# Kernel tuning notes

Measured on AMD Instinct MI355X. Metric: run time of the kernel, lower is better.

## Reference

```python
import jax, jax.numpy as jnp
import numpy as np

DEPTH, DIM, HEADS, DH, MLP, N, B = 6, 192, 12, 16, 768, 256, 32
INNER = HEADS * DH  # 192


def setup_inputs() -> dict:
    key = jax.random.key(0)
    ks = jax.random.split(key, 10)
    w = lambda i, shape: jax.random.normal(ks[i], shape, dtype=jnp.float32) * 0.02
    return {
        'x': jax.random.normal(ks[0], (B, N, DIM), dtype=jnp.float32),
        'ln1_g': jnp.ones((DEPTH, DIM), jnp.float32),
        'ln1_b': jnp.zeros((DEPTH, DIM), jnp.float32),
        'Wq': w(1, (DEPTH, DIM, INNER)),
        'Wkv': w(2, (DEPTH, DIM, 2 * INNER)),
        'lsa_scale': jnp.full((DEPTH, HEADS), DH ** -0.5, dtype=jnp.float32),
        'mix_pre': jax.random.normal(ks[3], (DEPTH, HEADS, HEADS), dtype=jnp.float32),
        'mix_post': jax.random.normal(ks[4], (DEPTH, HEADS, HEADS), dtype=jnp.float32),
        'Wo': w(5, (DEPTH, INNER, DIM)),
        'bo': jnp.zeros((DEPTH, DIM), jnp.float32),
        'ls1': jnp.full((DEPTH, DIM), 0.1, dtype=jnp.float32),
        'ln2_g': jnp.ones((DEPTH, DIM), jnp.float32),
        'ln2_b': jnp.zeros((DEPTH, DIM), jnp.float32),
        'W1': w(6, (DEPTH, DIM, MLP)),
        'b1': jnp.zeros((DEPTH, MLP), jnp.float32),
        'W2': w(7, (DEPTH, MLP, DIM)),
        'b2': jnp.zeros((DEPTH, DIM), jnp.float32),
        'ls2': jnp.full((DEPTH, DIM), 0.1, dtype=jnp.float32),
    }


def _ln(x, g, b, eps=1e-5):
    m = x.mean(-1, keepdims=True)
    v = ((x - m) ** 2).mean(-1, keepdims=True)
    return (x - m) * jax.lax.rsqrt(v + eps) * g + b


def _heads(t, b, n):
    # (b, n, h*d) -> (b, h, n, d)
    return t.reshape(b, n, HEADS, DH).transpose(0, 2, 1, 3)


def _forward(x, ln1_g, ln1_b, Wq, Wkv, lsa_scale, mix_pre, mix_post, Wo, bo,
             ls1, ln2_g, ln2_b, W1, b1, W2, b2, ls2):
    b, n, _ = x.shape
    diag = jnp.arange(n)
    for l in range(DEPTH):
        # --- PreNorm + talking-heads LSA attention + LayerScale(0.1) ---
        h = _ln(x, ln1_g[l], ln1_b[l])
        q = _heads(h @ Wq[l], b, n)
        k, v = jnp.split(h @ Wkv[l], 2, axis=-1)
        k, v = _heads(k, b, n), _heads(v, b, n)
        dots = jnp.einsum('bhid,bhjd->bhij', q, k) * lsa_scale[l][None, :, None, None]
        # LSA: source sets diagonal to -1e-09 (literal, near-zero) when if_patch_attn
        dots = dots.at[:, :, diag, diag].set(-1e-9)
        dots = jnp.einsum('bhij,hg->bgij', dots, mix_pre[l])
        a = jax.nn.softmax(dots, axis=-1)
        a = jnp.einsum('bhij,hg->bgij', a, mix_post[l])
        o = jnp.einsum('bhij,bhjd->bhid', a, v)
        o = o.transpose(0, 2, 1, 3).reshape(b, n, INNER) @ Wo[l] + bo[l]
        x = x + o * ls1[l]
        # --- PreNorm + GELU FFN + LayerScale(0.1) ---
        h2 = _ln(x, ln2_g[l], ln2_b[l])
        f = jax.nn.gelu(h2 @ W1[l] + b1[l], approximate=False) @ W2[l] + b2[l]
        x = x + f * ls2[l]
    return x


def reference(x, ln1_g, ln1_b, Wq, Wkv, lsa_scale, mix_pre, mix_post, Wo, bo,
              ls1, ln2_g, ln2_b, W1, b1, W2, b2, ls2):
    return _forward(x, ln1_g, ln1_b, Wq, Wkv, lsa_scale, mix_pre, mix_post, Wo,
                    bo, ls1, ln2_g, ln2_b, W1, b1, W2, b2, ls2)
```

## Files before the change

### kernel.cpp

```cpp
#include <hip/hip_runtime.h>
#include <hip/hip_bf16.h>

#define DEPTH   6
#define DIM     192
#define HEADS   12
#define DH      16
#define MLPD    768
#define SEQ     256
#define BATCH   32
#define ROWS    (BATCH*SEQ)

typedef __attribute__((ext_vector_type(8))) short short8;
typedef __attribute__((ext_vector_type(4))) float f32x4;
typedef __attribute__((ext_vector_type(4))) _Float16 half4;
typedef __attribute__((ext_vector_type(8))) _Float16 half8;
typedef __hip_bfloat16 bf16_t;
typedef _Float16 f16_t;

__device__ __forceinline__ bf16_t f2b(float v){ return __float2bfloat16(v); }
__device__ __forceinline__ ushort f2u(float v){
    union{ bf16_t b; ushort u; } w; w.b = __float2bfloat16(v); return w.u;
}
__device__ __forceinline__ f16_t u2h(ushort u){ union{ ushort u; f16_t h; } w; w.u = u; return w.h; }
__device__ __forceinline__ ushort h2u(f16_t h){ union{ ushort u; f16_t h; } w; w.h = h; return w.u; }

__device__ __forceinline__ void async16(ushort* lds, const ushort* gp){
    __builtin_amdgcn_global_load_lds(
        (const __attribute__((address_space(1))) uint*)gp,
        (__attribute__((address_space(3))) uint*)lds, 16, 0, 0);
}

__global__ void copy_kernel(const float* __restrict__ x, float* __restrict__ xr, int n){
    int i = blockIdx.x*256 + threadIdx.x;
    if (i < n) xr[i] = x[i];
}

__device__ __forceinline__ void wt_tile(const float* __restrict__ W,
        ushort* __restrict__ WT, int K, int N, int l, int tx, int ty,
        int tid, ushort* T){
    const float* src = W + ((size_t)l*K + tx*64)*N + ty*64;
    ushort* dst = WT + ((size_t)l*N + ty*64)*K + tx*64;
    int r = tid >> 2, c4 = (tid & 3)*16;
    #pragma unroll
    for (int u=0; u<4; u++){
        float4 v = *(const float4*)(src + (size_t)r*N + c4 + u*4);
        T[(c4+u*4+0)*72 + r] = f2u(v.x);
        T[(c4+u*4+1)*72 + r] = f2u(v.y);
        T[(c4+u*4+2)*72 + r] = f2u(v.z);
        T[(c4+u*4+3)*72 + r] = f2u(v.w);
    }
    __syncthreads();
    int n = tid >> 2, k8 = (tid & 3)*16;
    #pragma unroll
    for (int u=0; u<2; u++)
        *(uint4*)(dst + (size_t)n*K + k8 + u*8) = *(uint4*)&T[n*72 + k8 + u*8];
}

__global__ __launch_bounds__(256) void wt_all(
        const float* __restrict__ Wq, const float* __restrict__ Wkv,
        const float* __restrict__ Wo, const float* __restrict__ W1,
        const float* __restrict__ W2,
        ushort* __restrict__ WqT, ushort* __restrict__ WkvT,
        ushort* __restrict__ WoT, ushort* __restrict__ W1T,
        ushort* __restrict__ W2T){
    __shared__ ushort T[64*72];
    int id = blockIdx.x, l = blockIdx.y, tid = threadIdx.x;
    if (id < 9)       wt_tile(Wq,  WqT,  192, 192, l, id/3,       id%3,       tid, T);
    else if (id < 27) wt_tile(Wkv, WkvT, 192, 384, l, (id-9)/6,   (id-9)%6,   tid, T);
    else if (id < 36) wt_tile(Wo,  WoT,  192, 192, l, (id-27)/3,  (id-27)%3,  tid, T);
    else if (id < 72) wt_tile(W1,  W1T,  192, 768, l, (id-36)/12, (id-36)%12, tid, T);
    else              wt_tile(W2,  W2T,  768, 192, l, (id-72)/3,  (id-72)%3,  tid, T);
}

template<int MODE, int NT>
__global__ __launch_bounds__(256) void gemm_ln_kernel(
        const float* __restrict__ xres, const float* __restrict__ ln_g,
        const float* __restrict__ ln_b, const ushort* __restrict__ BT0,
        const ushort* __restrict__ BT1, const float* __restrict__ bias,
        f16_t* __restrict__ out0, f16_t* __restrict__ out1){
    __shared__ ushort As[64*200];
    __shared__ ushort Bs[2][6*2048];
    int tid = threadIdx.x, lane = tid & 63, w = tid >> 6;
    int bm = blockIdx.x*64;
    int tile0 = blockIdx.y*NT;
    auto issueB = [&](int t, int buf){
        int bn = (tile0 + t)*64;
        const ushort* bt; int bnl;
        if (MODE == 0 && bn >= DIM){ bt = BT1; bnl = bn - DIM; }
        else { bt = BT0; bnl = bn; }
        const ushort* bp = bt + (size_t)(bnl + (tid>>2))*DIM + (tid&3)*8;
        #pragma unroll
        for (int c=0; c<6; c++)
            async16(&Bs[buf][c*2048 + tid*8], bp + c*32);
    };
    issueB(0, 0);
    float g0 = ln_g[lane], g1 = ln_g[lane+64], g2 = ln_g[lane+128];
    float e0 = ln_b[lane], e1 = ln_b[lane+64], e2 = ln_b[lane+128];
    for (int it = 0; it < 16; it++){
        int r = (w<<4) + it;
        const float* xr = xres + (size_t)(bm + r)*DIM;
        float v0 = xr[lane], v1 = xr[lane+64], v2 = xr[lane+128];
        float s = v0+v1+v2;
        #pragma unroll
        for (int off=32; off; off>>=1) s += __shfl_xor(s, off, 64);
        float m = s*(1.0f/192.0f);
        float d0=v0-m, d1=v1-m, d2=v2-m;
        float q = d0*d0+d1*d1+d2*d2;
        #pragma unroll
        for (int off=32; off; off>>=1) q += __shfl_xor(q, off, 64);
        float inv = rsqrtf(q*(1.0f/192.0f) + 1e-5f);
        ushort* dst = &As[r*200];
        dst[lane]     = f2u(d0*inv*g0 + e0);
        dst[lane+64]  = f2u(d1*inv*g1 + e1);
        dst[lane+128] = f2u(d2*inv*g2 + e2);
    }
    __syncthreads();
    int wrow = w >> 1, wcol = w & 1;
    int quad = lane >> 4, mr = lane & 15;
    for (int t = 0; t < NT; t++){
        if (t+1 < NT) issueB(t+1, (t+1)&1);
        const ushort* B = Bs[t&1];
        f32x4 acc[2][2] = {};
        #pragma unroll
        for (int c = 0; c < 6; c++){
            short8 a0 = *(const short8*)&As[(wrow*32+mr)*200    + c*32 + quad*8];
            short8 a1 = *(const short8*)&As[(wrow*32+16+mr)*200 + c*32 + quad*8];
            short8 b0 = *(const short8*)&B[c*2048 + (wcol*32+mr)*32    + quad*8];
            short8 b1 = *(const short8*)&B[c*2048 + (wcol*32+16+mr)*32 + quad*8];
            acc[0][0] = __builtin_amdgcn_mfma_f32_16x16x32_bf16(a0, b0, acc[0][0], 0,0,0);
            acc[0][1] = __builtin_amdgcn_mfma_f32_16x16x32_bf16(a0, b1, acc[0][1], 0,0,0);
            acc[1][0] = __builtin_amdgcn_mfma_f32_16x16x32_bf16(a1, b0, acc[1][0], 0,0,0);
            acc[1][1] = __builtin_amdgcn_mfma_f32_16x16x32_bf16(a1, b1, acc[1][1], 0,0,0);
        }
        int bn = (tile0 + t)*64;
        #pragma unroll
        for (int rr=0; rr<2; rr++){
            #pragma unroll
            for (int cc=0; cc<2; cc++){
                int col = bn + wcol*32 + cc*16 + mr;
                if (MODE == 0){
                    f16_t* op; size_t st;
                    if (col < DIM){ op = out0 + col; st = DIM; }
                    else          { op = out1 + (col - DIM); st = 2*DIM; }
                    #pragma unroll
                    for (int tt=0; tt<4; tt++){
                        int row = bm + wrow*32 + rr*16 + quad*4 + tt;
                        op[(size_t)row*st] = (f16_t)acc[rr][cc][tt];
                    }
                } else {
                    float bv = bias[col];
                    #pragma unroll
                    for (int tt=0; tt<4; tt++){
                        int row = bm + wrow*32 + rr*16 + quad*4 + tt;
                        float z = acc[rr][cc][tt] + bv;
                        ((bf16_t*)out0)[(size_t)row*MLPD + col] =
                            f2b(0.5f*z*(1.0f + erff(z*0.70710678118654752f)));
                    }
                }
            }
        }
        __syncthreads();
    }
}

template<int ROUNDS>
__global__ __launch_bounds__(256) void gemm_a_kernel(
        const ushort* __restrict__ A, const ushort* __restrict__ BT,
        const float* __restrict__ bias, const float* __restrict__ ls,
        float* __restrict__ xres){
    const int K = ROUNDS*192;
    __shared__ ushort As[6*2048];
    __shared__ ushort Bs[6*2048];
    int tid = threadIdx.x, lane = tid & 63, w = tid >> 6;
    int wrow = w >> 1, wcol = w & 1;
    int bm = blockIdx.x*64, bn = blockIdx.y*64;
    int quad = lane >> 4, mr = lane & 15;
    const ushort* ap = A  + (size_t)(bm + (tid>>2))*K + (tid&3)*8;
    const ushort* bp = BT + (size_t)(bn + (tid>>2))*K + (tid&3)*8;
    f32x4 acc[2][2] = {};
    for (int r = 0; r < ROUNDS; r++){
        #pragma unroll
        for (int c=0; c<6; c++){
            async16(&As[c*2048 + tid*8], ap + r*192 + c*32);
            async16(&Bs[c*2048 + tid*8], bp + r*192 + c*32);
        }
        __syncthreads();
        #pragma unroll
        for (int c=0; c<6; c++){
            short8 a0 = *(const short8*)&As[c*2048 + (wrow*32+mr)*32    + quad*8];
            short8 a1 = *(const short8*)&As[c*2048 + (wrow*32+16+mr)*32 + quad*8];
            short8 b0 = *(const short8*)&Bs[c*2048 + (wcol*32+mr)*32    + quad*8];
            short8 b1 = *(const short8*)&Bs[c*2048 + (wcol*32+16+mr)*32 + quad*8];
            acc[0][0] = __builtin_amdgcn_mfma_f32_16x16x32_bf16(a0, b0, acc[0][0], 0,0,0);
            acc[0][1] = __builtin_amdgcn_mfma_f32_16x16x32_bf16(a0, b1, acc[0][1], 0,0,0);
            acc[1][0] = __builtin_amdgcn_mfma_f32_16x16x32_bf16(a1, b0, acc[1][0], 0,0,0);
            acc[1][1] = __builtin_amdgcn_mfma_f32_16x16x32_bf16(a1, b1, acc[1][1], 0,0,0);
        }
        if (r+1 < ROUNDS) __syncthreads();
    }
    #pragma unroll
    for (int rr=0; rr<2; rr++){
        #pragma unroll
        for (int cc=0; cc<2; cc++){
            int col = bn + wcol*32 + cc*16 + mr;
            float bv = bias[col], lv = ls[col];
            #pragma unroll
            for (int tt=0; tt<4; tt++){
                int row = bm + wrow*32 + rr*16 + quad*4 + tt;
                xres[(size_t)row*DIM + col] += (acc[rr][cc][tt] + bv)*lv;
            }
        }
    }
}

#define SLAB    4488
#define IST     280
#define KV_OFF  53856
#define ROWP    200
#define Q_OFF   66656
#define POST_OFF 70112
#define PRE_OFF 71776
#define LTOT    71920

__global__ __launch_bounds__(1024, 1) void attn_kernel(
        const f16_t* __restrict__ qb, const f16_t* __restrict__ kvb,
        const float* __restrict__ lsa, const float* __restrict__ pre,
        const float* __restrict__ post, const ushort* __restrict__ WoT,
        const float* __restrict__ bo, const float* __restrict__ ls1,
        float* __restrict__ xres){
    __shared__ ushort L[LTOT];
    int tid  = threadIdx.x;
    int lane = tid & 63, w = tid >> 6;
    int quad = lane >> 4, nr = lane & 15;
    int b  = blockIdx.x >> 4;
    int i0 = (blockIdx.x & 15) << 4;

    {
        uint* Z = (uint*)&L[KV_OFF];
        for (int k = tid; k < (LTOT - KV_OFF)/2; k += 1024) Z[k] = 0;
    }
    __syncthreads();

    if (tid < 384){
        int e = tid*8, i = e/DIM, d = e%DIM, hh = d >> 4;
        float sc = lsa[hh];
        union { uint4 v; f16_t h[8]; } iv, ov;
        iv.v = *(const uint4*)(qb + (size_t)(b*SEQ + i0 + i)*DIM + d);
        #pragma unroll
        for (int u=0; u<8; u++) ov.h[u] = (f16_t)((float)iv.h[u]*sc);
        *(uint4*)&L[Q_OFF + i*ROWP + d] = ov.v;
    } else if (tid < 512){
        for (int k = tid-384; k < 256; k += 128){
            int gg = k >> 4, hh = k & 15;
            if (gg < 12 && hh < 12)
                L[POST_OFF + k] = h2u((f16_t)post[hh*12+gg]);
        }
    } else if (tid < 640){
        for (int k = tid-512; k < 144; k += 128)
            L[PRE_OFF + k] = h2u((f16_t)pre[k]);
    }
    auto stage_kv = [&](int c, int coloff){
        for (int u = tid; u < 1536; u += 1024){
            int e = u*8;
            int j = e/DIM, d = e%DIM;
            uint4 v = *(const uint4*)(kvb + (size_t)(b*SEQ + c*64 + j)*(2*DIM) + coloff + d);
            *(uint4*)&L[KV_OFF + j*ROWP + d] = v;
        }
    };
    __syncthreads();

    half4 postTf = *(const half4*)&L[POST_OFF + nr*16 + quad*4];

    {
        int jg = w*16 + nr;
        const f16_t* krow = kvb + (size_t)(b*SEQ + jg)*(2*DIM);
        half8 qh[6], kh[6];
        #pragma unroll
        for (int c=0; c<6; c++){
            union{ short8 s; half8 h; } a, k2;
            a.s  = *(const short8*)&L[Q_OFF + nr*ROWP + c*32 + quad*8];
            k2.s = *(const short8*)(const void*)(krow + c*32 + quad*8);
            qh[c] = a.h; kh[c] = k2.h;
        }
        int dd = jg - (i0 + quad*4);
        int hb = (quad>>1)*12;
        #pragma unroll
        for (int g=0; g<12; g++){
            f32x4 a = {0,0,0,0};
            #pragma unroll
            for (int c=0; c<6; c++){
                f16_t s = u2h(L[PRE_OFF + hb + c*24 + g]);
                a = __builtin_amdgcn_mfma_f32_16x16x32_f16(qh[c]*s, kh[c], a, 0,0,0);
            }
            ushort* sp = &L[g*SLAB + jg];
            sp[(quad*4+0)*IST] = (dd==0) ? (ushort)0 : h2u((f16_t)a[0]);
            sp[(quad*4+1)*IST] = (dd==1) ? (ushort)0 : h2u((f16_t)a[1]);
            sp[(quad*4+2)*IST] = (dd==2) ? (ushort)0 : h2u((f16_t)a[2]);
            sp[(quad*4+3)*IST] = (dd==3) ? (ushort)0 : h2u((f16_t)a[3]);
        }
    }
    __syncthreads();

    for (int r = w; r < 192; r += 16){
        int g = r >> 4, i = r & 15;
        ushort* sp = &L[g*SLAB + i*IST];
        ushort4 uv = *(ushort4*)&sp[lane*4];
        float e0 = __expf((float)u2h(uv.x));
        float e1 = __expf((float)u2h(uv.y));
        float e2 = __expf((float)u2h(uv.z));
        float e3 = __expf((float)u2h(uv.w));
        float ssum = e0+e1+e2+e3;
        #pragma unroll
        for (int off=32; off; off>>=1) ssum += __shfl_xor(ssum, off, 64);
        float rin = 1.0f/ssum;
        uv.x = h2u((f16_t)(e0*rin)); uv.y = h2u((f16_t)(e1*rin));
        uv.z = h2u((f16_t)(e2*rin)); uv.w = h2u((f16_t)(e3*rin));
        *(ushort4*)&sp[lane*4] = uv;
    }
    __syncthreads();

    for (int s = 0; s < 16; s++){
        int cb = s*16 + w;
        int i = cb >> 4, jb = cb & 15;
        int colbase = i*IST + jb*16 + nr;
        half4 bv;
        #pragma unroll
        for (int t=0; t<4; t++) bv[t] = u2h(L[(quad*4+t)*SLAB + colbase]);
        f32x4 cc = __builtin_amdgcn_mfma_f32_16x16x16f16(postTf, bv, (f32x4){0,0,0,0}, 0,0,0);
        if (quad < 3){
            #pragma unroll
            for (int t=0; t<4; t++) L[(quad*4+t)*SLAB + colbase] = h2u((f16_t)cc[t]);
        }
    }
    __syncthreads();

    f32x4 oacc = {0,0,0,0};
    for (int c = 0; c < 4; c++){
        stage_kv(c, DIM);
        __syncthreads();
        if (w < 12){
            int g = w;
            #pragma unroll
            for (int ks = 0; ks < 4; ks++){
                int jl = ks*16 + quad*4;
                half4 av = *(const half4*)&L[g*SLAB + nr*IST + c*64 + jl];
                half4 bv;
                #pragma unroll
                for (int t=0; t<4; t++) bv[t] = u2h(L[KV_OFF + (jl+t)*ROWP + g*16 + nr]);
                oacc = __builtin_amdgcn_mfma_f32_16x16x16f16(av, bv, oacc, 0,0,0);
            }
        }
        __syncthreads();
    }

    if (w < 12){
        int g = w;
        #pragma unroll
        for (int t=0; t<4; t++){
            int i = quad*4 + t;
            L[Q_OFF + i*ROWP + g*16 + nr] = f2u(oacc[t]);
        }
    }
    __syncthreads();

    if (w < 12){
        f32x4 wacc = {0,0,0,0};
        int ct = w;
        const ushort* wg = WoT + (size_t)(ct*16 + nr)*192;
        #pragma unroll
        for (int c = 0; c < 3; c++){
            #pragma unroll
            for (int sub = 0; sub < 2; sub++){
                int k0 = c*64 + sub*32;
                short8 av = *(const short8*)&L[Q_OFF + nr*ROWP + k0 + quad*8];
                short8 bv = *(const short8*)(wg + k0 + quad*8);
                wacc = __builtin_amdgcn_mfma_f32_16x16x32_bf16(av, bv, wacc, 0,0,0);
            }
        }
        int col = ct*16 + nr;
        float bv2 = bo[col], lv = ls1[col];
        #pragma unroll
        for (int t=0; t<4; t++){
            int row = b*SEQ + i0 + quad*4 + t;
            xres[(size_t)row*DIM + col] += (wacc[t] + bv2)*lv;
        }
    }
}

extern "C" void kernel_launch(void* const* d_in, const int* in_sizes, int n_in,
                              void* d_out, int out_size, void* d_ws, size_t ws_size,
                              hipStream_t stream){
    const float* x    = (const float*)d_in[0];
    const float* ln1g = (const float*)d_in[1];
    const float* ln1b = (const float*)d_in[2];
    const float* Wq   = (const float*)d_in[3];
    const float* Wkv  = (const float*)d_in[4];
    const float* lsa  = (const float*)d_in[5];
    const float* pre  = (const float*)d_in[6];
    const float* post = (const float*)d_in[7];
    const float* Wo   = (const float*)d_in[8];
    const float* bo   = (const float*)d_in[9];
    const float* ls1  = (const float*)d_in[10];
    const float* ln2g = (const float*)d_in[11];
    const float* ln2b = (const float*)d_in[12];
    const float* W1   = (const float*)d_in[13];
    const float* b1   = (const float*)d_in[14];
    const float* W2   = (const float*)d_in[15];
    const float* b2   = (const float*)d_in[16];
    const float* ls2  = (const float*)d_in[17];
    float* xres = (float*)d_out;

    char* ws = (char*)d_ws;
    f16_t*  qb  = (f16_t*)ws;
    f16_t*  kvb = (f16_t*)(ws + (size_t)ROWS*DIM*2);
    bf16_t* fb  = (bf16_t*)ws;
    char* p = ws + (size_t)ROWS*MLPD*2;
    ushort* WqT  = (ushort*)p; p += (size_t)DEPTH*DIM*DIM*2;
    ushort* WkvT = (ushort*)p; p += (size_t)DEPTH*DIM*2*DIM*2;
    ushort* WoT  = (ushort*)p; p += (size_t)DEPTH*DIM*DIM*2;
    ushort* W1T  = (ushort*)p; p += (size_t)DEPTH*DIM*MLPD*2;
    ushort* W2T  = (ushort*)p; p += (size_t)DEPTH*MLPD*DIM*2;

    int ntot = ROWS*DIM;
    copy_kernel<<<ntot/256, 256, 0, stream>>>(x, xres, ntot);
    wt_all<<<dim3(108, 6), 256, 0, stream>>>(Wq, Wkv, Wo, W1, W2,
                                             WqT, WkvT, WoT, W1T, W2T);
    for (int l = 0; l < DEPTH; l++){
        gemm_ln_kernel<0,3><<<dim3(128,3), 256, 0, stream>>>(xres,
                ln1g + l*DIM, ln1b + l*DIM,
                WqT + (size_t)l*DIM*DIM, WkvT + (size_t)l*DIM*2*DIM,
                nullptr, qb, kvb);
        attn_kernel<<<BATCH*(SEQ/16), 1024, 0, stream>>>(qb, kvb, lsa + l*HEADS,
                pre + l*HEADS*HEADS, post + l*HEADS*HEADS,
                WoT + (size_t)l*DIM*DIM, bo + l*DIM, ls1 + l*DIM, xres);
        gemm_ln_kernel<1,4><<<dim3(128,3), 256, 0, stream>>>(xres,
                ln2g + l*DIM, ln2b + l*DIM,
                W1T + (size_t)l*DIM*MLPD, nullptr, b1 + l*MLPD, (f16_t*)fb, nullptr);
        gemm_a_kernel<4><<<dim3(128,3), 256, 0, stream>>>((const ushort*)fb,
                W2T + (size_t)l*MLPD*DIM, b2 + l*DIM, ls2 + l*DIM, xres);
    }
}
```

Before: 703.9 us.

## Split LayerNorm into its own kernel and halve attention query tile

Moves LayerNorm out of the two GEMM kernels into a standalone kernel that writes bf16 normalized rows to a workspace buffer. The GEMMs then load A tiles with async copies, so each of the three column-blocks no longer recomputes LN. The attention kernel now handles 8 query rows per block instead of 16, which roughly halves LDS use and raises the occupancy hint to 8. It also stages V in 32-row chunks with a register prefetch of the next chunk. The trade-offs are two extra launches and an extra global round trip per layer, plus wasted MFMA lanes, since the 16-row MFMA tiles now carry only 8 valid rows.

```diff
diff --git a/kernel.cpp b/kernel.cpp
--- a/kernel.cpp
+++ b/kernel.cpp
@@ -72,13 +72,36 @@
     else              wt_tile(W2,  W2T,  768, 192, l, (id-72)/3,  (id-72)%3,  tid, T);
 }
 
+__global__ __launch_bounds__(256) void ln_kernel(
+        const float* __restrict__ xres, const float* __restrict__ ln_g,
+        const float* __restrict__ ln_b, ushort* __restrict__ out){
+    int lane = threadIdx.x & 63, w = threadIdx.x >> 6;
+    int row = blockIdx.x*4 + w;
+    const float* xr = xres + (size_t)row*DIM;
+    float v0 = xr[lane], v1 = xr[lane+64], v2 = xr[lane+128];
+    float s = v0+v1+v2;
+    #pragma unroll
+    for (int off=32; off; off>>=1) s += __shfl_xor(s, off, 64);
+    float m = s*(1.0f/192.0f);
+    float d0=v0-m, d1=v1-m, d2=v2-m;
+    float q = d0*d0+d1*d1+d2*d2;
+    #pragma unroll
+    for (int off=32; off; off>>=1) q += __shfl_xor(q, off, 64);
+    float inv = rsqrtf(q*(1.0f/192.0f) + 1e-5f);
+    float g0 = ln_g[lane], g1 = ln_g[lane+64], g2 = ln_g[lane+128];
+    float e0 = ln_b[lane], e1 = ln_b[lane+64], e2 = ln_b[lane+128];
+    ushort* dst = out + (size_t)row*DIM;
+    dst[lane]     = f2u(d0*inv*g0 + e0);
+    dst[lane+64]  = f2u(d1*inv*g1 + e1);
+    dst[lane+128] = f2u(d2*inv*g2 + e2);
+}
+
 template<int MODE, int NT>
 __global__ __launch_bounds__(256) void gemm_ln_kernel(
-        const float* __restrict__ xres, const float* __restrict__ ln_g,
-        const float* __restrict__ ln_b, const ushort* __restrict__ BT0,
+        const ushort* __restrict__ Aln, const ushort* __restrict__ BT0,
         const ushort* __restrict__ BT1, const float* __restrict__ bias,
         f16_t* __restrict__ out0, f16_t* __restrict__ out1){
-    __shared__ ushort As[64*200];
+    __shared__ ushort As[6*2048];
     __shared__ ushort Bs[2][6*2048];
     int tid = threadIdx.x, lane = tid & 63, w = tid >> 6;
     int bm = blockIdx.x*64;
@@ -93,27 +116,13 @@
         for (int c=0; c<6; c++)
             async16(&Bs[buf][c*2048 + tid*8], bp + c*32);
     };
+    {
+        const ushort* ap = Aln + (size_t)(bm + (tid>>2))*DIM + (tid&3)*8;
+        #pragma unroll
+        for (int c=0; c<6; c++)
+            async16(&As[c*2048 + tid*8], ap + c*32);
+    }
     issueB(0, 0);
-    float g0 = ln_g[lane], g1 = ln_g[lane+64], g2 = ln_g[lane+128];
-    float e0 = ln_b[lane], e1 = ln_b[lane+64], e2 = ln_b[lane+128];
-    for (int it = 0; it < 16; it++){
-        int r = (w<<4) + it;
-        const float* xr = xres + (size_t)(bm + r)*DIM;
-        float v0 = xr[lane], v1 = xr[lane+64], v2 = xr[lane+128];
-        float s = v0+v1+v2;
-        #pragma unroll
-        for (int off=32; off; off>>=1) s += __shfl_xor(s, off, 64);
-        float m = s*(1.0f/192.0f);
-        float d0=v0-m, d1=v1-m, d2=v2-m;
-        float q = d0*d0+d1*d1+d2*d2;
-        #pragma unroll
-        for (int off=32; off; off>>=1) q += __shfl_xor(q, off, 64);
-        float inv = rsqrtf(q*(1.0f/192.0f) + 1e-5f);
-        ushort* dst = &As[r*200];
-        dst[lane]     = f2u(d0*inv*g0 + e0);
-        dst[lane+64]  = f2u(d1*inv*g1 + e1);
-        dst[lane+128] = f2u(d2*inv*g2 + e2);
-    }
     __syncthreads();
     int wrow = w >> 1, wcol = w & 1;
     int quad = lane >> 4, mr = lane & 15;
@@ -123,8 +132,8 @@
         f32x4 acc[2][2] = {};
         #pragma unroll
         for (int c = 0; c < 6; c++){
-            short8 a0 = *(const short8*)&As[(wrow*32+mr)*200    + c*32 + quad*8];
-            short8 a1 = *(const short8*)&As[(wrow*32+16+mr)*200 + c*32 + quad*8];
+            short8 a0 = *(const short8*)&As[c*2048 + (wrow*32+mr)*32    + quad*8];
+            short8 a1 = *(const short8*)&As[c*2048 + (wrow*32+16+mr)*32 + quad*8];
             short8 b0 = *(const short8*)&B[c*2048 + (wcol*32+mr)*32    + quad*8];
             short8 b1 = *(const short8*)&B[c*2048 + (wcol*32+16+mr)*32 + quad*8];
             acc[0][0] = __builtin_amdgcn_mfma_f32_16x16x32_bf16(a0, b0, acc[0][0], 0,0,0);
@@ -213,16 +222,16 @@
     }
 }
 
-#define SLAB    4488
-#define IST     280
-#define KV_OFF  53856
-#define ROWP    200
-#define Q_OFF   66656
-#define POST_OFF 70112
-#define PRE_OFF 71776
-#define LTOT    71920
-
-__global__ __launch_bounds__(1024, 1) void attn_kernel(
+#define IST      280
+#define SLAB     2248
+#define KV_OFF   26976
+#define ROWP     200
+#define Q_OFF    35968
+#define POST_OFF 39168
+#define PRE_OFF  39424
+#define LTOT     39568
+
+__global__ __launch_bounds__(1024, 8) void attn_kernel(
         const f16_t* __restrict__ qb, const f16_t* __restrict__ kvb,
         const float* __restrict__ lsa, const float* __restrict__ pre,
         const float* __restrict__ post, const ushort* __restrict__ WoT,
@@ -232,16 +241,16 @@
     int tid  = threadIdx.x;
     int lane = tid & 63, w = tid >> 6;
     int quad = lane >> 4, nr = lane & 15;
-    int b  = blockIdx.x >> 4;
-    int i0 = (blockIdx.x & 15) << 4;
+    int b  = blockIdx.x >> 5;
+    int i0 = (blockIdx.x & 31) << 3;
 
     {
         uint* Z = (uint*)&L[KV_OFF];
-        for (int k = tid; k < (LTOT - KV_OFF)/2; k += 1024) Z[k] = 0;
-    }
-    __syncthreads();
-
-    if (tid < 384){
+        for (int k = tid; k < (16*SLAB - KV_OFF)/2; k += 1024) Z[k] = 0;
+    }
+    __syncthreads();
+
+    if (tid < 192){
         int e = tid*8, i = e/DIM, d = e%DIM, hh = d >> 4;
         float sc = lsa[hh];
         union { uint4 v; f16_t h[8]; } iv, ov;
@@ -249,24 +258,16 @@
         #pragma unroll
         for (int u=0; u<8; u++) ov.h[u] = (f16_t)((float)iv.h[u]*sc);
         *(uint4*)&L[Q_OFF + i*ROWP + d] = ov.v;
-    } else if (tid < 512){
-        for (int k = tid-384; k < 256; k += 128){
+    } else if (tid < 320){
+        for (int k = tid-192; k < 256; k += 128){
             int gg = k >> 4, hh = k & 15;
-            if (gg < 12 && hh < 12)
-                L[POST_OFF + k] = h2u((f16_t)post[hh*12+gg]);
-        }
-    } else if (tid < 640){
-        for (int k = tid-512; k < 144; k += 128)
+            L[POST_OFF + k] = (gg < 12 && hh < 12) ? h2u((f16_t)post[hh*12+gg])
+                                                   : (ushort)0;
+        }
+    } else if (tid < 448){
+        for (int k = tid-320; k < 144; k += 128)
             L[PRE_OFF + k] = h2u((f16_t)pre[k]);
     }
-    auto stage_kv = [&](int c, int coloff){
-        for (int u = tid; u < 1536; u += 1024){
-            int e = u*8;
-            int j = e/DIM, d = e%DIM;
-            uint4 v = *(const uint4*)(kvb + (size_t)(b*SEQ + c*64 + j)*(2*DIM) + coloff + d);
-            *(uint4*)&L[KV_OFF + j*ROWP + d] = v;
-        }
-    };
     __syncthreads();
 
     half4 postTf = *(const half4*)&L[POST_OFF + nr*16 + quad*4];
@@ -292,17 +293,19 @@
                 f16_t s = u2h(L[PRE_OFF + hb + c*24 + g]);
                 a = __builtin_amdgcn_mfma_f32_16x16x32_f16(qh[c]*s, kh[c], a, 0,0,0);
             }
-            ushort* sp = &L[g*SLAB + jg];
-            sp[(quad*4+0)*IST] = (dd==0) ? (ushort)0 : h2u((f16_t)a[0]);
-            sp[(quad*4+1)*IST] = (dd==1) ? (ushort)0 : h2u((f16_t)a[1]);
-            sp[(quad*4+2)*IST] = (dd==2) ? (ushort)0 : h2u((f16_t)a[2]);
-            sp[(quad*4+3)*IST] = (dd==3) ? (ushort)0 : h2u((f16_t)a[3]);
-        }
-    }
-    __syncthreads();
-
-    for (int r = w; r < 192; r += 16){
-        int g = r >> 4, i = r & 15;
+            if (quad < 2){
+                ushort* sp = &L[g*SLAB + jg];
+                sp[(quad*4+0)*IST] = (dd==0) ? (ushort)0 : h2u((f16_t)a[0]);
+                sp[(quad*4+1)*IST] = (dd==1) ? (ushort)0 : h2u((f16_t)a[1]);
+                sp[(quad*4+2)*IST] = (dd==2) ? (ushort)0 : h2u((f16_t)a[2]);
+                sp[(quad*4+3)*IST] = (dd==3) ? (ushort)0 : h2u((f16_t)a[3]);
+            }
+        }
+    }
+    __syncthreads();
+
+    for (int r = w; r < 96; r += 16){
+        int g = r >> 3, i = r & 7;
         ushort* sp = &L[g*SLAB + i*IST];
         ushort4 uv = *(ushort4*)&sp[lane*4];
         float e0 = __expf((float)u2h(uv.x));
@@ -319,7 +322,7 @@
     }
     __syncthreads();
 
-    for (int s = 0; s < 16; s++){
+    for (int s = 0; s < 8; s++){
         int cb = s*16 + w;
         int i = cb >> 4, jb = cb & 15;
         int colbase = i*IST + jb*16 + nr;
@@ -335,15 +338,26 @@
     __syncthreads();
 
     f32x4 oacc = {0,0,0,0};
-    for (int c = 0; c < 4; c++){
-        stage_kv(c, DIM);
+    {
+        if (tid < 768){
+            int e = tid*8, j = e/192, d = e - j*192;
+            uint4 v = *(const uint4*)(kvb + (size_t)(b*SEQ + j)*(2*DIM) + DIM + d);
+            *(uint4*)&L[KV_OFF + j*ROWP + d] = v;
+        }
         __syncthreads();
+    }
+    for (int c = 0; c < 8; c++){
+        uint4 pv; int pj = 0, pd = 0;
+        if (c+1 < 8 && tid < 768){
+            int e = tid*8; pj = e/192; pd = e - pj*192;
+            pv = *(const uint4*)(kvb + (size_t)(b*SEQ + (c+1)*32 + pj)*(2*DIM) + DIM + pd);
+        }
         if (w < 12){
             int g = w;
             #pragma unroll
-            for (int ks = 0; ks < 4; ks++){
+            for (int ks = 0; ks < 2; ks++){
                 int jl = ks*16 + quad*4;
-                half4 av = *(const half4*)&L[g*SLAB + nr*IST + c*64 + jl];
+                half4 av = *(const half4*)&L[g*SLAB + nr*IST + c*32 + jl];
                 half4 bv;
                 #pragma unroll
                 for (int t=0; t<4; t++) bv[t] = u2h(L[KV_OFF + (jl+t)*ROWP + g*16 + nr]);
@@ -351,9 +365,12 @@
             }
         }
         __syncthreads();
-    }
-
-    if (w < 12){
+        if (c+1 < 8 && tid < 768)
+            *(uint4*)&L[KV_OFF + pj*ROWP + pd] = pv;
+        __syncthreads();
+    }
+
+    if (w < 12 && quad < 2){
         int g = w;
         #pragma unroll
         for (int t=0; t<4; t++){
@@ -377,12 +394,14 @@
                 wacc = __builtin_amdgcn_mfma_f32_16x16x32_bf16(av, bv, wacc, 0,0,0);
             }
         }
-        int col = ct*16 + nr;
-        float bv2 = bo[col], lv = ls1[col];
-        #pragma unroll
-        for (int t=0; t<4; t++){
-            int row = b*SEQ + i0 + quad*4 + t;
-            xres[(size_t)row*DIM + col] += (wacc[t] + bv2)*lv;
+        if (quad < 2){
+            int col = ct*16 + nr;
+            float bv2 = bo[col], lv = ls1[col];
+            #pragma unroll
+            for (int t=0; t<4; t++){
+                int row = b*SEQ + i0 + quad*4 + t;
+                xres[(size_t)row*DIM + col] += (wacc[t] + bv2)*lv;
+            }
         }
     }
 }
@@ -420,21 +439,22 @@
     ushort* WoT  = (ushort*)p; p += (size_t)DEPTH*DIM*DIM*2;
     ushort* W1T  = (ushort*)p; p += (size_t)DEPTH*DIM*MLPD*2;
     ushort* W2T  = (ushort*)p; p += (size_t)DEPTH*MLPD*DIM*2;
+    ushort* lnb  = (ushort*)p; p += (size_t)ROWS*DIM*2;
 
     int ntot = ROWS*DIM;
     copy_kernel<<<ntot/256, 256, 0, stream>>>(x, xres, ntot);
     wt_all<<<dim3(108, 6), 256, 0, stream>>>(Wq, Wkv, Wo, W1, W2,
                                              WqT, WkvT, WoT, W1T, W2T);
     for (int l = 0; l < DEPTH; l++){
-        gemm_ln_kernel<0,3><<<dim3(128,3), 256, 0, stream>>>(xres,
-                ln1g + l*DIM, ln1b + l*DIM,
+        ln_kernel<<<ROWS/4, 256, 0, stream>>>(xres, ln1g + l*DIM, ln1b + l*DIM, lnb);
+        gemm_ln_kernel<0,3><<<dim3(128,3), 256, 0, stream>>>(lnb,
                 WqT + (size_t)l*DIM*DIM, WkvT + (size_t)l*DIM*2*DIM,
                 nullptr, qb, kvb);
-        attn_kernel<<<BATCH*(SEQ/16), 1024, 0, stream>>>(qb, kvb, lsa + l*HEADS,
+        attn_kernel<<<BATCH*(SEQ/8), 1024, 0, stream>>>(qb, kvb, lsa + l*HEADS,
                 pre + l*HEADS*HEADS, post + l*HEADS*HEADS,
                 WoT + (size_t)l*DIM*DIM, bo + l*DIM, ls1 + l*DIM, xres);
-        gemm_ln_kernel<1,4><<<dim3(128,3), 256, 0, stream>>>(xres,
-                ln2g + l*DIM, ln2b + l*DIM,
+        ln_kernel<<<ROWS/4, 256, 0, stream>>>(xres, ln2g + l*DIM, ln2b + l*DIM, lnb);
+        gemm_ln_kernel<1,4><<<dim3(128,3), 256, 0, stream>>>(lnb,
                 W1T + (size_t)l*DIM*MLPD, nullptr, b1 + l*MLPD, (f16_t*)fb, nullptr);
         gemm_a_kernel<4><<<dim3(128,3), 256, 0, stream>>>((const ushort*)fb,
                 W2T + (size_t)l*MLPD*DIM, b2 + l*DIM, ls2 + l*DIM, xres);
```

After: 723.9 us. +2.8%, slower.
